# Optimization experiments

Measured on AMD Instinct MI355X. Metric: run time of the kernel, lower is better.

The kernel has to match this reference:

```python
import jax, jax.numpy as jnp
import numpy as np

EPS = 1e-6
NEG_SLOPE = 0.2


def setup_inputs() -> dict:
    key = jax.random.key(0)
    k1, k2 = jax.random.split(key)
    B, D, T = 4, 512, 2048
    H, Dh = 8, 512 // 8
    x = jax.random.normal(k1, (B, D, T), dtype=jnp.float32)
    qkv = jax.random.normal(k2, (3, H, D, Dh), dtype=jnp.float32) * 0.02
    norm_w = jnp.ones((1,), dtype=jnp.float32)
    return {"x": x, "qkv": qkv, "norm_w": norm_w}


def reference(x, qkv, norm_w):
    B, D, T = x.shape
    H = qkv.shape[1]
    # leaky relu on channels-first input
    x = jnp.where(x >= 0, x, NEG_SLOPE * x)
    # fused QKV projection: (B,D,T),(3,H,D,Dh) -> (3,B,H,T,Dh)
    h = jnp.einsum('bdt,nhdD->nbhtD', x, qkv)
    # RMSNorm over the sequence axis (dim=-2), scalar learned weight
    denom = jnp.mean(h * h, axis=-2, keepdims=True)
    h = norm_w * (h / jnp.sqrt(denom + EPS))
    q, k, v = h[0], h[1], h[2]
    scale = jnp.sqrt(jnp.asarray(D // H, dtype=x.dtype))
    # manual attention: (B,H,T,T) score matrix
    attn = jax.nn.softmax(jnp.einsum('bhtD,bhTD->bhtT', q, k) / scale, axis=-1)
    # weighted values, output laid out (B,H,Dh,T) then merged to (B,D,T)
    out = jnp.einsum('bhtT,bhTD->bhDt', attn, v)
    return out.reshape(B, D, T)
```

## Files before the change

kernel.cpp:

```cpp
#include <hip/hip_runtime.h>
#include <cstddef>

#define B   4
#define D   512
#define T   2048
#define H   8
#define DH  64
#define NEG_SLOPE 0.2f
#define EPS 1e-6f
#define LOG2E 1.44269504088896340736f

typedef __attribute__((ext_vector_type(8))) short short8;
typedef __attribute__((ext_vector_type(4))) float float4v;
typedef __attribute__((ext_vector_type(2))) int   int2v;

__device__ __forceinline__ float bf2f(ushort u) {
    unsigned int x = ((unsigned int)u) << 16;
    return __builtin_bit_cast(float, x);
}
__device__ __forceinline__ ushort f2bf(float f) {
    unsigned int x = __builtin_bit_cast(unsigned int, f);
    x = x + 0x7fffu + ((x >> 16) & 1u);
    return (ushort)(x >> 16);
}

#define GLD16(gptr, lptr) __builtin_amdgcn_global_load_lds( \
    (const __attribute__((address_space(1))) unsigned int*)(gptr), \
    (__attribute__((address_space(3))) unsigned int*)(lptr), 16, 0, 0)

__global__ __launch_bounds__(256) void transpose_both(const float* __restrict__ x,
                                                      ushort* __restrict__ xT,
                                                      const float* __restrict__ qkv,
                                                      ushort* __restrict__ WT,
                                                      float* __restrict__ ssq, int zcount) {
    const int tid = threadIdx.x;
    const int bid = blockIdx.x;

    const float* src; ushort* dst;
    int src_ld, dst_ld, do_lrelu, bx, by, bz;
    size_t src_ms, dst_ms;
    if (bid < 1024) {
        bx = bid & 31; by = (bid >> 5) & 7; bz = bid >> 8;
        src = x; dst = xT; src_ld = T; dst_ld = D;
        src_ms = (size_t)D * T; dst_ms = (size_t)T * D; do_lrelu = 1;
        if (bid == 0) for (int i = tid; i < zcount; i += 256) ssq[i] = 0.f;
    } else {
        int wb = bid - 1024;
        bx = 0; by = wb & 7; bz = wb >> 3;
        src = qkv; dst = WT; src_ld = DH; dst_ld = D;
        src_ms = (size_t)D * DH; dst_ms = (size_t)DH * D; do_lrelu = 0;
    }

    const int c0 = bx * 64, r0 = by * 64;
    const float* s = src + bz * src_ms + (size_t)r0 * src_ld + c0;
    ushort*      d = dst + bz * dst_ms + (size_t)c0 * dst_ld + r0;

    __shared__ float Ls[64][68];

    const int rl = tid >> 4, c4 = (tid & 15) * 4;
    #pragma unroll
    for (int p = 0; p < 4; ++p) {
        float4 v = *(const float4*)(s + (size_t)(rl + p * 16) * src_ld + c4);
        if (do_lrelu) {
            v.x = fmaxf(v.x, NEG_SLOPE * v.x);
            v.y = fmaxf(v.y, NEG_SLOPE * v.y);
            v.z = fmaxf(v.z, NEG_SLOPE * v.z);
            v.w = fmaxf(v.w, NEG_SLOPE * v.w);
        }
        *(float4*)&Ls[rl + p * 16][c4] = v;
    }
    __syncthreads();

    const int tl = tid >> 2;
    #pragma unroll
    for (int it = 0; it < 2; ++it) {
        int ch = (tid & 3) + it * 4;
        ushort o[8];
        #pragma unroll
        for (int j = 0; j < 8; ++j) o[j] = f2bf(Ls[ch * 8 + j][tl]);
        *(uint4*)(d + (size_t)tl * dst_ld + ch * 8) = *(uint4*)o;
    }
}

__global__ __launch_bounds__(256, 5) void qkv_mm(const ushort* __restrict__ xT,
                                                 const ushort* __restrict__ WT,
                                                 ushort* __restrict__ hb,
                                                 ushort* __restrict__ vT,
                                                 float* __restrict__ ssq) {
    const int tid = threadIdx.x, wave = tid >> 6, lane = tid & 63;
    const int quad = lane >> 4, l16 = lane & 15;
    const int wr = wave >> 1, wc = wave & 1;
    const int t0  = blockIdx.x * 64;
    const int gd0 = blockIdx.y * 128;
    const int b   = blockIdx.z;

    __shared__ ushort At[64 * 64];
    __shared__ ushort Bt[128 * 64];

    const ushort* xb = xT + (size_t)b * T * D + (size_t)t0 * D;
    const ushort* wb = WT + (size_t)gd0 * D;

    const int srow = lane >> 3;
    const int csrc = (lane & 7) ^ srow;

    float4v acc[2][4];
    #pragma unroll
    for (int i = 0; i < 2; ++i)
        #pragma unroll
        for (int j = 0; j < 4; ++j) acc[i][j] = (float4v){0.f, 0.f, 0.f, 0.f};

    for (int k0 = 0; k0 < D; k0 += 64) {
        #pragma unroll
        for (int i = 0; i < 2; ++i) {
            int rbase = wave * 16 + i * 8;
            GLD16(xb + (size_t)(rbase + srow) * D + k0 + csrc * 8, &At[rbase * 64]);
        }
        #pragma unroll
        for (int i = 0; i < 4; ++i) {
            int rbase = wave * 32 + i * 8;
            GLD16(wb + (size_t)(rbase + srow) * D + k0 + csrc * 8, &Bt[rbase * 64]);
        }
        __syncthreads();

        #pragma unroll
        for (int kh = 0; kh < 2; ++kh) {
            short8 aF[2], bF[4];
            #pragma unroll
            for (int mt = 0; mt < 2; ++mt) {
                int row = wr * 32 + mt * 16 + l16;
                aF[mt] = *(const short8*)&At[row * 64 + (((kh * 4 + quad) ^ (l16 & 7)) * 8)];
            }
            #pragma unroll
            for (int nt = 0; nt < 4; ++nt) {
                int row = wc * 64 + nt * 16 + l16;
                bF[nt] = *(const short8*)&Bt[row * 64 + (((kh * 4 + quad) ^ (l16 & 7)) * 8)];
            }
            #pragma unroll
            for (int mt = 0; mt < 2; ++mt)
                #pragma unroll
                for (int nt = 0; nt < 4; ++nt)
                    acc[mt][nt] = __builtin_amdgcn_mfma_f32_16x16x32_bf16(
                        aF[mt], bF[nt], acc[mt][nt], 0, 0, 0);
        }
        __syncthreads();
    }

    const int g = blockIdx.y * 2 + wc;
    const int n = g >> 3, hh = g & 7;
    float colsq[4] = {0.f, 0.f, 0.f, 0.f};

    if (n < 2) {
        ushort* hbase = hb + (((size_t)n * B + b) * H + hh) * (size_t)T * DH;
        #pragma unroll
        for (int mt = 0; mt < 2; ++mt) {
            #pragma unroll
            for (int nt = 0; nt < 4; ++nt) {
                float4v c = acc[mt][nt];
                int dd = nt * 16 + l16;
                #pragma unroll
                for (int r = 0; r < 4; ++r) {
                    int t = t0 + wr * 32 + mt * 16 + quad * 4 + r;
                    hbase[(size_t)t * DH + dd] = f2bf(c[r]);
                    colsq[nt] += c[r] * c[r];
                }
            }
        }
    } else {
        ushort* vbase = vT + ((size_t)b * H + hh) * (size_t)DH * T;
        #pragma unroll
        for (int mt = 0; mt < 2; ++mt) {
            #pragma unroll
            for (int nt = 0; nt < 4; ++nt) {
                float4v c = acc[mt][nt];
                int dd = nt * 16 + l16;
                int t  = t0 + wr * 32 + mt * 16 + quad * 4;
                ushort4 pk;
                pk.x = f2bf(c[0]); pk.y = f2bf(c[1]);
                pk.z = f2bf(c[2]); pk.w = f2bf(c[3]);
                *(ushort4*)(vbase + (size_t)dd * T + t) = pk;
                colsq[nt] += c[0]*c[0] + c[1]*c[1] + c[2]*c[2] + c[3]*c[3];
            }
        }
    }
    #pragma unroll
    for (int nt = 0; nt < 4; ++nt) {
        float s = colsq[nt];
        s += __shfl_xor(s, 16);
        s += __shfl_xor(s, 32);
        if (quad == 0)
            atomicAdd(&ssq[(((size_t)n * B + b) * H + hh) * 64 + nt * 16 + l16], s);
    }
}

__global__ __launch_bounds__(256, 4) void flash_attn(const ushort* __restrict__ hb,
                                                     const ushort* __restrict__ vT,
                                                     const float* __restrict__ ssq,
                                                     const float* __restrict__ norm_w,
                                                     float* __restrict__ out) {
    const int tid  = threadIdx.x;
    const int wave = tid >> 6;
    const int lane = tid & 63;
    const int quad = lane >> 4;
    const int l16  = lane & 15;

    const int lin  = blockIdx.x;
    const int head = ((lin & 7) << 2) | ((lin >> 3) & 3);
    const int t0   = (lin >> 5) * 64;
    const int b    = head >> 3, hh = head & 7;

    const size_t slab = (size_t)B * H * T * DH;
    const ushort* qp = hb + (size_t)head * T * DH;
    const ushort* kp = hb + slab + (size_t)head * T * DH;
    const ushort* vp = vT + (size_t)head * DH * T;

    __shared__ ushort Kt[2][64 * 64];
    __shared__ ushort Vt[64 * 64];
    __shared__ float fqk[64], sv[64];

    if (tid < 64) {
        float nw = norm_w[0];
        float mq = ssq[(0 * B * H + head) * 64 + tid] * (1.0f / T) + EPS;
        float mk = ssq[(1 * B * H + head) * 64 + tid] * (1.0f / T) + EPS;
        float mv = ssq[(2 * B * H + head) * 64 + tid] * (1.0f / T) + EPS;
        fqk[tid] = nw * nw * rsqrtf(mq) * rsqrtf(mk) * 0.125f * LOG2E;
        sv[tid]  = nw * rsqrtf(mv);
    }

    const int srow = lane >> 3;
    const int csrc = (lane & 7) ^ srow;
    const ushort* kA = kp + (size_t)(wave * 16 + srow) * DH + csrc * 8;
    const ushort* kB = kp + (size_t)(wave * 16 + 8 + srow) * DH + csrc * 8;
    const ushort* vA = vp + (size_t)(wave * 16 + srow) * T + csrc * 8;
    const ushort* vB = vp + (size_t)(wave * 16 + 8 + srow) * T + csrc * 8;

    GLD16(kA, &Kt[0][(wave * 16) * 64]);
    GLD16(kB, &Kt[0][(wave * 16 + 8) * 64]);

    __syncthreads();
    short8 bQ[2];
    {
        const ushort* qr = qp + (size_t)(t0 + wave * 16 + l16) * DH;
        #pragma unroll
        for (int kh = 0; kh < 2; ++kh) {
            short8 raw = *(const short8*)(qr + kh * 32 + quad * 8);
            #pragma unroll
            for (int j = 0; j < 8; ++j) {
                float f = bf2f((ushort)raw[j]) * fqk[kh * 32 + quad * 8 + j];
                bQ[kh][j] = (short)f2bf(f);
            }
        }
    }

    float l_run = 0.f;
    float4v O[4];
    #pragma unroll
    for (int dt = 0; dt < 4; ++dt) O[dt] = (float4v){0.f, 0.f, 0.f, 0.f};

    int cur = 0;
    for (int j0 = 0; j0 < T; j0 += 64) {
        GLD16(vA + j0, &Vt[(wave * 16) * 64]);
        GLD16(vB + j0, &Vt[(wave * 16 + 8) * 64]);

        if (j0 + 64 < T) {
            GLD16(kA + (size_t)(j0 + 64) * DH, &Kt[cur ^ 1][(wave * 16) * 64]);
            GLD16(kB + (size_t)(j0 + 64) * DH, &Kt[cur ^ 1][(wave * 16 + 8) * 64]);
        }

        float4v S[4];
        #pragma unroll
        for (int mt = 0; mt < 4; ++mt) S[mt] = (float4v){0.f, 0.f, 0.f, 0.f};
        #pragma unroll
        for (int kh = 0; kh < 2; ++kh) {
            #pragma unroll
            for (int mt = 0; mt < 4; ++mt) {
                int row = mt * 16 + l16;
                short8 aK = *(const short8*)&Kt[cur][row * 64 + (((kh * 4 + quad) ^ (l16 & 7)) * 8)];
                S[mt] = __builtin_amdgcn_mfma_f32_16x16x32_bf16(aK, bQ[kh], S[mt], 0, 0, 0);
            }
        }

        int2v pP[4];
        #pragma unroll
        for (int mt = 0; mt < 4; ++mt) {
            float p0 = __builtin_amdgcn_exp2f(S[mt][0]);
            float p1 = __builtin_amdgcn_exp2f(S[mt][1]);
            float p2 = __builtin_amdgcn_exp2f(S[mt][2]);
            float p3 = __builtin_amdgcn_exp2f(S[mt][3]);
            l_run += (p0 + p1) + (p2 + p3);
            unsigned int a0 = __builtin_bit_cast(unsigned int, p0) + 0x8000u;
            unsigned int a1 = __builtin_bit_cast(unsigned int, p1) + 0x8000u;
            unsigned int a2 = __builtin_bit_cast(unsigned int, p2) + 0x8000u;
            unsigned int a3 = __builtin_bit_cast(unsigned int, p3) + 0x8000u;
            pP[mt][0] = (int)__builtin_amdgcn_perm(a1, a0, 0x07060302u);
            pP[mt][1] = (int)__builtin_amdgcn_perm(a3, a2, 0x07060302u);
        }

        __syncthreads();

        #pragma unroll
        for (int mt = 0; mt < 4; ++mt) {
            #pragma unroll
            for (int dt = 0; dt < 4; ++dt) {
                int row = dt * 16 + l16;
                int2v av = *(const int2v*)&Vt[row * 64
                               + (((mt * 2 + (quad >> 1)) ^ (row & 7)) * 8)
                               + (quad & 1) * 4];
                asm("v_mfma_f32_16x16x16_bf16 %0, %1, %2, %0"
                    : "+v"(O[dt]) : "v"(av), "v"(pP[mt]));
            }
        }

        __syncthreads();
        cur ^= 1;
    }

    float rs = l_run;
    rs += __shfl_xor(rs, 16);
    rs += __shfl_xor(rs, 32);
    float inv = 1.f / rs;
    const int t = t0 + wave * 16 + l16;
    #pragma unroll
    for (int dt = 0; dt < 4; ++dt) {
        #pragma unroll
        for (int r = 0; r < 4; ++r) {
            int dd = dt * 16 + quad * 4 + r;
            out[((size_t)b * D + hh * DH + dd) * T + t] = O[dt][r] * inv * sv[dd];
        }
    }
}

extern "C" void kernel_launch(void* const* d_in, const int* in_sizes, int n_in,
                              void* d_out, int out_size, void* d_ws, size_t ws_size,
                              hipStream_t stream) {
    const float* x      = (const float*)d_in[0];
    const float* qkv    = (const float*)d_in[1];
    const float* norm_w = (const float*)d_in[2];
    float* out = (float*)d_out;

    const size_t HB_BYTES = (size_t)2 * B * H * T * DH * 2;
    const size_t VT_BYTES = (size_t)B * H * DH * T * 2;
    const size_t XT_BYTES = (size_t)B * T * D * 2;
    const size_t WT_BYTES = (size_t)3 * H * DH * D * 2;
    ushort* hb  = (ushort*)d_ws;
    ushort* vT  = (ushort*)((char*)d_ws + HB_BYTES);
    ushort* xT  = (ushort*)((char*)d_ws + HB_BYTES + VT_BYTES);
    ushort* WT  = (ushort*)((char*)d_ws + HB_BYTES + VT_BYTES + XT_BYTES);
    float*  ssq = (float*)((char*)d_ws + HB_BYTES + VT_BYTES + XT_BYTES + WT_BYTES);
    const int SSQ_N = 3 * B * H * DH;

    transpose_both<<<dim3(1024 + 192), 256, 0, stream>>>(x, xT, qkv, WT, ssq, SSQ_N);

    qkv_mm<<<dim3(T / 64, (3 * H * DH) / 128, B), 256, 0, stream>>>(xT, WT, hb, vT, ssq);
    flash_attn<<<dim3((T / 64) * B * H), 256, 0, stream>>>(hb, vT, ssq, norm_w, out);
}
```

Baseline: 154.4 us.

## Split attention KV range into two halves and merge with a reduce kernel

```diff
diff --git a/kernel.cpp b/kernel.cpp
--- a/kernel.cpp
+++ b/kernel.cpp
@@ -6,6 +6,7 @@
 #define T   2048
 #define H   8
 #define DH  64
+#define BH  32
 #define NEG_SLOPE 0.2f
 #define EPS 1e-6f
 #define LOG2E 1.44269504088896340736f
@@ -196,7 +197,8 @@
                                                      const ushort* __restrict__ vT,
                                                      const float* __restrict__ ssq,
                                                      const float* __restrict__ norm_w,
-                                                     float* __restrict__ out) {
+                                                     ushort* __restrict__ op,
+                                                     float* __restrict__ lp) {
     const int tid  = threadIdx.x;
     const int wave = tid >> 6;
     const int lane = tid & 63;
@@ -204,9 +206,11 @@
     const int l16  = lane & 15;
 
     const int lin  = blockIdx.x;
-    const int head = ((lin & 7) << 2) | ((lin >> 3) & 3);
-    const int t0   = (lin >> 5) * 64;
-    const int b    = head >> 3, hh = head & 7;
+    const int l10  = lin & 1023;
+    const int half = lin >> 10;
+    const int head = ((l10 & 7) << 2) | ((l10 >> 3) & 3);
+    const int t0   = (l10 >> 5) * 64;
+    const int h0   = half * 1024;
 
     const size_t slab = (size_t)B * H * T * DH;
     const ushort* qp = hb + (size_t)head * T * DH;
@@ -215,23 +219,21 @@
 
     __shared__ ushort Kt[2][64 * 64];
     __shared__ ushort Vt[64 * 64];
-    __shared__ float fqk[64], sv[64];
+    __shared__ float fqk[64];
 
     if (tid < 64) {
         float nw = norm_w[0];
         float mq = ssq[(0 * B * H + head) * 64 + tid] * (1.0f / T) + EPS;
         float mk = ssq[(1 * B * H + head) * 64 + tid] * (1.0f / T) + EPS;
-        float mv = ssq[(2 * B * H + head) * 64 + tid] * (1.0f / T) + EPS;
         fqk[tid] = nw * nw * rsqrtf(mq) * rsqrtf(mk) * 0.125f * LOG2E;
-        sv[tid]  = nw * rsqrtf(mv);
     }
 
     const int srow = lane >> 3;
     const int csrc = (lane & 7) ^ srow;
-    const ushort* kA = kp + (size_t)(wave * 16 + srow) * DH + csrc * 8;
-    const ushort* kB = kp + (size_t)(wave * 16 + 8 + srow) * DH + csrc * 8;
-    const ushort* vA = vp + (size_t)(wave * 16 + srow) * T + csrc * 8;
-    const ushort* vB = vp + (size_t)(wave * 16 + 8 + srow) * T + csrc * 8;
+    const ushort* kA = kp + (size_t)(h0 + wave * 16 + srow) * DH + csrc * 8;
+    const ushort* kB = kp + (size_t)(h0 + wave * 16 + 8 + srow) * DH + csrc * 8;
+    const ushort* vA = vp + (size_t)(wave * 16 + srow) * T + h0 + csrc * 8;
+    const ushort* vB = vp + (size_t)(wave * 16 + 8 + srow) * T + h0 + csrc * 8;
 
     GLD16(kA, &Kt[0][(wave * 16) * 64]);
     GLD16(kB, &Kt[0][(wave * 16 + 8) * 64]);
@@ -257,11 +259,11 @@
     for (int dt = 0; dt < 4; ++dt) O[dt] = (float4v){0.f, 0.f, 0.f, 0.f};
 
     int cur = 0;
-    for (int j0 = 0; j0 < T; j0 += 64) {
+    for (int j0 = 0; j0 < 1024; j0 += 64) {
         GLD16(vA + j0, &Vt[(wave * 16) * 64]);
         GLD16(vB + j0, &Vt[(wave * 16 + 8) * 64]);
 
-        if (j0 + 64 < T) {
+        if (j0 + 64 < 1024) {
             GLD16(kA + (size_t)(j0 + 64) * DH, &Kt[cur ^ 1][(wave * 16) * 64]);
             GLD16(kB + (size_t)(j0 + 64) * DH, &Kt[cur ^ 1][(wave * 16 + 8) * 64]);
         }
@@ -317,16 +319,49 @@
     float rs = l_run;
     rs += __shfl_xor(rs, 16);
     rs += __shfl_xor(rs, 32);
-    float inv = 1.f / rs;
     const int t = t0 + wave * 16 + l16;
+    ushort* opb = op + ((size_t)half * BH + head) * (size_t)DH * T;
     #pragma unroll
     for (int dt = 0; dt < 4; ++dt) {
         #pragma unroll
         for (int r = 0; r < 4; ++r) {
             int dd = dt * 16 + quad * 4 + r;
-            out[((size_t)b * D + hh * DH + dd) * T + t] = O[dt][r] * inv * sv[dd];
-        }
-    }
+            opb[(size_t)dd * T + t] = f2bf(O[dt][r]);
+        }
+    }
+    if (quad == 0)
+        lp[((size_t)half * BH + head) * T + t] = rs;
+}
+
+__global__ __launch_bounds__(256) void reduce_out(const ushort* __restrict__ op,
+                                                  const float* __restrict__ lp,
+                                                  const float* __restrict__ ssq,
+                                                  const float* __restrict__ norm_w,
+                                                  float* __restrict__ out) {
+    const size_t g0 = ((size_t)blockIdx.x * 256 + threadIdx.x) * 8;
+    const int head = (int)(g0 >> 17);
+    const int rem  = (int)(g0 & 131071);
+    const int dd   = rem >> 11;
+    const int t    = rem & 2047;
+
+    const size_t HS = (size_t)BH * DH * T;
+    uint4 u0 = *(const uint4*)(op + g0);
+    uint4 u1 = *(const uint4*)(op + HS + g0);
+    const ushort* p0 = (const ushort*)&u0;
+    const ushort* p1 = (const ushort*)&u1;
+
+    const float* la = lp + (size_t)head * T + t;
+    const float* lb = lp + (size_t)BH * T + (size_t)head * T + t;
+
+    float sv = norm_w[0] * rsqrtf(ssq[(2 * BH + head) * 64 + dd] * (1.0f / T) + EPS);
+
+    float o[8];
+    #pragma unroll
+    for (int i = 0; i < 8; ++i)
+        o[i] = (bf2f(p0[i]) + bf2f(p1[i])) * sv / (la[i] + lb[i]);
+
+    *(float4*)(out + g0)     = *(float4*)&o[0];
+    *(float4*)(out + g0 + 4) = *(float4*)&o[4];
 }
 
 extern "C" void kernel_launch(void* const* d_in, const int* in_sizes, int n_in,
@@ -341,15 +376,23 @@
     const size_t VT_BYTES = (size_t)B * H * DH * T * 2;
     const size_t XT_BYTES = (size_t)B * T * D * 2;
     const size_t WT_BYTES = (size_t)3 * H * DH * D * 2;
-    ushort* hb  = (ushort*)d_ws;
-    ushort* vT  = (ushort*)((char*)d_ws + HB_BYTES);
-    ushort* xT  = (ushort*)((char*)d_ws + HB_BYTES + VT_BYTES);
-    ushort* WT  = (ushort*)((char*)d_ws + HB_BYTES + VT_BYTES + XT_BYTES);
-    float*  ssq = (float*)((char*)d_ws + HB_BYTES + VT_BYTES + XT_BYTES + WT_BYTES);
+    const size_t SSQ_BYTES = (size_t)3 * B * H * DH * 4;
+    const size_t LP_BYTES  = (size_t)2 * BH * T * 4;
+    char* w = (char*)d_ws;
+    ushort* hb  = (ushort*)w;                                  w += HB_BYTES;
+    ushort* vT  = (ushort*)w;                                  w += VT_BYTES;
+    ushort* xT  = (ushort*)w;                                  w += XT_BYTES;
+    ushort* WT  = (ushort*)w;                                  w += WT_BYTES;
+    float*  ssq = (float*)w;                                   w += SSQ_BYTES;
+    float*  lp  = (float*)w;                                   w += LP_BYTES;
+    ushort* op  = (ushort*)w;
     const int SSQ_N = 3 * B * H * DH;
 
     transpose_both<<<dim3(1024 + 192), 256, 0, stream>>>(x, xT, qkv, WT, ssq, SSQ_N);
 
     qkv_mm<<<dim3(T / 64, (3 * H * DH) / 128, B), 256, 0, stream>>>(xT, WT, hb, vT, ssq);
-    flash_attn<<<dim3((T / 64) * B * H), 256, 0, stream>>>(hb, vT, ssq, norm_w, out);
-}
+
+    flash_attn<<<dim3(2048), 256, 0, stream>>>(hb, vT, ssq, norm_w, op, lp);
+
+    reduce_out<<<dim3(2048), 256, 0, stream>>>(op, lp, ssq, norm_w, out);
+}
```

After: 161.1 us. 1.04x slower.
